# Kernel tuning notes

Measured on AMD Instinct MI355X. Metric: run time of the kernel, lower is better.

The kernel has to match this reference:

```python
import jax, jax.numpy as jnp
import numpy as np

B, D, K = 4096, 512, 64


def setup_inputs() -> dict:
    key = jax.random.key(0)
    k1, k2, k3, k4, k5, k6 = jax.random.split(key, 6)
    observations = jax.random.normal(k1, (B, D), dtype=jnp.float32)
    # binary mask (1 = observed, 0 = missing), stored as float for multiply
    mask = jnp.round(jax.random.uniform(k2, (B, D), dtype=jnp.float32))
    F = jax.random.normal(k3, (1, D, 10), dtype=jnp.float32) * 0.1
    b = jax.random.normal(k4, (1, D, 1), dtype=jnp.float32) * 0.1
    W = jax.random.normal(k5, (11, K), dtype=jnp.float32) * 0.1
    bw = jax.random.normal(k6, (K,), dtype=jnp.float32) * 0.1
    return {"observations": observations, "mask": mask, "F": F, "b": b, "W": W, "bw": bw}


def reference(observations, mask, F, b, W, bw):
    # x_aug per (batch, feature): [x*F_d (10), b_d (1)] -> 11-dim
    Bn = observations.shape[0]
    xF = observations[:, :, None] * F[0]                      # [B, D, 10]
    b_bc = jnp.broadcast_to(b[0], (observations.shape[1], 1)) # [D, 1]
    aug = jnp.concatenate([xF, jnp.broadcast_to(b_bc, (Bn,) + b_bc.shape)], axis=-1)  # [B, D, 11]
    encoded = jnp.einsum('bdf,fk->bdk', aug, W) + bw          # [B, D, K]
    out = jax.nn.relu(jnp.sum(encoded * mask[:, :, None], axis=1))  # [B, K]
    return out
```

## Files before the change

### kernel.cpp

```cpp
#include <hip/hip_runtime.h>
#include <hip/hip_bf16.h>


#define D_DIM 512
#define K_DIM 64
#define B_DIM 4096

typedef __attribute__((ext_vector_type(4))) float f32x4;
typedef __attribute__((ext_vector_type(8))) short bf16x8;

__device__ __forceinline__ unsigned short f2bf(float f) {
    unsigned u = __builtin_bit_cast(unsigned, f);
    u += 0x7fffu + ((u >> 16) & 1u);
    return (unsigned short)(u >> 16);
}

__global__ void prep_Gf_kernel(const float* __restrict__ F,
                               const float* __restrict__ W,
                               unsigned short* __restrict__ Gf) {
    int i = blockIdx.x * blockDim.x + threadIdx.x;
    int lane = i & 63;
    int tp   = (i >> 6) & 15;
    int w    = i >> 10;
    int n     = w * 16 + (lane & 15);
    int dbase = tp * 32 + (lane >> 4) * 8;
    unsigned short v[8];
#pragma unroll
    for (int j = 0; j < 8; ++j) {
        int d = dbase + j;
        float s = 0.f;
#pragma unroll
        for (int f = 0; f < 10; ++f)
            s = fmaf(F[d * 10 + f], W[f * 64 + n], s);
        v[j] = f2bf(s);
    }
    *reinterpret_cast<ushort4*>(Gf + (size_t)i * 8)     = make_ushort4(v[0], v[1], v[2], v[3]);
    *reinterpret_cast<ushort4*>(Gf + (size_t)i * 8 + 4) = make_ushort4(v[4], v[5], v[6], v[7]);
}

__global__ __launch_bounds__(256, 2)
void main_kernel(const float* __restrict__ obs,
                 const float* __restrict__ mask,
                 const float* __restrict__ bvec,
                 const float* __restrict__ W,
                 const float* __restrict__ bw,
                 const unsigned short* __restrict__ Gf,
                 float* __restrict__ out) {
    __shared__ __align__(16) unsigned short Xs[8 * 512];
    __shared__ float s0s[8], s1s[8];

    const int tid  = threadIdx.x;
    const int lane = tid & 63;
    const int w    = tid >> 6;
    const int rowbase = blockIdx.x * 8;

    bf16x8 gfr[16];
#pragma unroll
    for (int tp = 0; tp < 16; ++tp)
        gfr[tp] = *reinterpret_cast<const bf16x8*>(
            Gf + ((size_t)((w * 16 + tp) * 64 + lane)) * 8);

    const int kk = w * 16 + (lane & 15);
    const float w10 = W[10 * K_DIM + kk];
    const float bwv = bw[kk];

    {
        const int r = tid >> 5;
        const int c = tid & 31;
        const float* orow = obs  + (size_t)(rowbase + r) * D_DIM;
        const float* mrow = mask + (size_t)(rowbase + r) * D_DIM;
        f32x4 o[4], m[4], bv[4];
#pragma unroll
        for (int j = 0; j < 4; ++j) {
            int d = c * 4 + 128 * j;
            o[j]  = *reinterpret_cast<const f32x4*>(orow + d);
            m[j]  = *reinterpret_cast<const f32x4*>(mrow + d);
            bv[j] = *reinterpret_cast<const f32x4*>(bvec + d);
        }
        float p0 = 0.f, p1 = 0.f;
        const int swz = r << 4;
        char* xb = reinterpret_cast<char*>(Xs);
#pragma unroll
        for (int j = 0; j < 4; ++j) {
            ushort4 pk;
            pk.x = f2bf(o[j].x * m[j].x);
            pk.y = f2bf(o[j].y * m[j].y);
            pk.z = f2bf(o[j].z * m[j].z);
            pk.w = f2bf(o[j].w * m[j].w);
            int byteoff = r * 1024 + ((c * 8 + 256 * j) ^ swz);
            *reinterpret_cast<ushort4*>(xb + byteoff) = pk;
            p0 += (m[j].x + m[j].y) + (m[j].z + m[j].w);
            p1 = fmaf(m[j].x, bv[j].x, p1);
            p1 = fmaf(m[j].y, bv[j].y, p1);
            p1 = fmaf(m[j].z, bv[j].z, p1);
            p1 = fmaf(m[j].w, bv[j].w, p1);
        }
#pragma unroll
        for (int s = 1; s <= 16; s <<= 1) {
            p0 += __shfl_xor(p0, s, 64);
            p1 += __shfl_xor(p1, s, 64);
        }
        if (c == 0) { s0s[r] = p0; s1s[r] = p1; }
    }
    __syncthreads();

    f32x4 acc = {0.f, 0.f, 0.f, 0.f};
    {
        const int arow = lane & 7;
        const int g    = lane >> 4;
        const char* xb = reinterpret_cast<const char*>(Xs);
#pragma unroll
        for (int tp = 0; tp < 16; ++tp) {
            int byteoff = arow * 1024 + ((64 * tp + 16 * g) ^ (arow << 4));
            bf16x8 a = *reinterpret_cast<const bf16x8*>(xb + byteoff);
            acc = __builtin_amdgcn_mfma_f32_16x16x32_bf16(a, gfr[tp], acc, 0, 0, 0);
        }
    }

    if (lane < 32) {
        const int g = lane >> 4;
#pragma unroll
        for (int r = 0; r < 4; ++r) {
            const int rowl = g * 4 + r;
            float tot = acc[r];
            tot = fmaf(s1s[rowl], w10, tot);
            tot = fmaf(s0s[rowl], bwv, tot);
            out[(size_t)(rowbase + rowl) * K_DIM + kk] = fmaxf(tot, 0.f);
        }
    }
}

extern "C" void kernel_launch(void* const* d_in, const int* in_sizes, int n_in,
                              void* d_out, int out_size, void* d_ws, size_t ws_size,
                              hipStream_t stream) {
    const float* obs  = (const float*)d_in[0];
    const float* mask = (const float*)d_in[1];
    const float* F    = (const float*)d_in[2];
    const float* bvec = (const float*)d_in[3];
    const float* W    = (const float*)d_in[4];
    const float* bw   = (const float*)d_in[5];
    float* out = (float*)d_out;
    unsigned short* Gf = (unsigned short*)d_ws;

    prep_Gf_kernel<<<16, 256, 0, stream>>>(F, W, Gf);
    main_kernel<<<B_DIM / 8, 256, 0, stream>>>(obs, mask, bvec, W, bw, Gf, out);
}
```

Before: 13.16 us.

## Fuse Gf precompute into main kernel using per-block MFMA into LDS

Removes the separate prep kernel launch. Each block now recomputes the F·W product (512x64) itself with small MFMAs and stores it as bf16 in a 64KB LDS buffer. The main MFMA loop then reads its B operand from LDS instead of registers. This saves a launch and a global round-trip, but repeats the precompute in all 512 blocks. The larger LDS footprint may also cut occupancy.

```diff
diff --git a/kernel.cpp b/kernel.cpp
--- a/kernel.cpp
+++ b/kernel.cpp
@@ -14,81 +14,100 @@
     u += 0x7fffu + ((u >> 16) & 1u);
     return (unsigned short)(u >> 16);
 }
-
-__global__ void prep_Gf_kernel(const float* __restrict__ F,
-                               const float* __restrict__ W,
-                               unsigned short* __restrict__ Gf) {
-    int i = blockIdx.x * blockDim.x + threadIdx.x;
-    int lane = i & 63;
-    int tp   = (i >> 6) & 15;
-    int w    = i >> 10;
-    int n     = w * 16 + (lane & 15);
-    int dbase = tp * 32 + (lane >> 4) * 8;
-    unsigned short v[8];
-#pragma unroll
-    for (int j = 0; j < 8; ++j) {
-        int d = dbase + j;
-        float s = 0.f;
-#pragma unroll
-        for (int f = 0; f < 10; ++f)
-            s = fmaf(F[d * 10 + f], W[f * 64 + n], s);
-        v[j] = f2bf(s);
-    }
-    *reinterpret_cast<ushort4*>(Gf + (size_t)i * 8)     = make_ushort4(v[0], v[1], v[2], v[3]);
-    *reinterpret_cast<ushort4*>(Gf + (size_t)i * 8 + 4) = make_ushort4(v[4], v[5], v[6], v[7]);
+__device__ __forceinline__ unsigned pack2(float a, float b) {
+    return (unsigned)f2bf(a) | ((unsigned)f2bf(b) << 16);
 }
 
 __global__ __launch_bounds__(256, 2)
-void main_kernel(const float* __restrict__ obs,
-                 const float* __restrict__ mask,
-                 const float* __restrict__ bvec,
-                 const float* __restrict__ W,
-                 const float* __restrict__ bw,
-                 const unsigned short* __restrict__ Gf,
-                 float* __restrict__ out) {
-    __shared__ __align__(16) unsigned short Xs[8 * 512];
+void fused_kernel(const float* __restrict__ obs,
+                  const float* __restrict__ mask,
+                  const float* __restrict__ bvec,
+                  const float* __restrict__ F,
+                  const float* __restrict__ W,
+                  const float* __restrict__ bw,
+                  float* __restrict__ out) {
+    __shared__ __align__(16) unsigned short GF[4096 * 8];
+    __shared__ __align__(16) unsigned short XF[512 * 8];
     __shared__ float s0s[8], s1s[8];
 
     const int tid  = threadIdx.x;
     const int lane = tid & 63;
     const int w    = tid >> 6;
+    const int ln   = lane & 15;
+    const int g    = lane >> 4;
     const int rowbase = blockIdx.x * 8;
 
-    bf16x8 gfr[16];
+    const int r = tid >> 5;
+    const int c = tid & 31;
+    const float* orow = obs  + (size_t)(rowbase + r) * D_DIM;
+    const float* mrow = mask + (size_t)(rowbase + r) * D_DIM;
+    f32x4 o[4], m[4], bv[4];
 #pragma unroll
-    for (int tp = 0; tp < 16; ++tp)
-        gfr[tp] = *reinterpret_cast<const bf16x8*>(
-            Gf + ((size_t)((w * 16 + tp) * 64 + lane)) * 8);
-
-    const int kk = w * 16 + (lane & 15);
-    const float w10 = W[10 * K_DIM + kk];
-    const float bwv = bw[kk];
+    for (int j = 0; j < 4; ++j) {
+        int d = c * 4 + 128 * j;
+        o[j]  = *reinterpret_cast<const f32x4*>(orow + d);
+        m[j]  = *reinterpret_cast<const f32x4*>(mrow + d);
+        bv[j] = *reinterpret_cast<const f32x4*>(bvec + d);
+    }
 
     {
-        const int r = tid >> 5;
-        const int c = tid & 31;
-        const float* orow = obs  + (size_t)(rowbase + r) * D_DIM;
-        const float* mrow = mask + (size_t)(rowbase + r) * D_DIM;
-        f32x4 o[4], m[4], bv[4];
+        bf16x8 wf[4];
+#pragma unroll
+        for (int nt = 0; nt < 4; ++nt) {
+#pragma unroll
+            for (int j = 0; j < 8; ++j) {
+                int k = g * 8 + j;
+                wf[nt][j] = (k < 10)
+                    ? (short)f2bf(W[k * K_DIM + nt * 16 + ln]) : (short)0;
+            }
+        }
+#pragma unroll
+        for (int i = 0; i < 8; ++i) {
+            const int dt = w * 8 + i;
+            const int Frow = dt * 16 + ln;
+            const float* Fr = F + (size_t)Frow * 10;
+            float fa[8] = {0.f, 0.f, 0.f, 0.f, 0.f, 0.f, 0.f, 0.f};
+            if (g == 0) {
+                float2 t0 = *reinterpret_cast<const float2*>(Fr + 0);
+                float2 t1 = *reinterpret_cast<const float2*>(Fr + 2);
+                float2 t2 = *reinterpret_cast<const float2*>(Fr + 4);
+                float2 t3 = *reinterpret_cast<const float2*>(Fr + 6);
+                fa[0] = t0.x; fa[1] = t0.y; fa[2] = t1.x; fa[3] = t1.y;
+                fa[4] = t2.x; fa[5] = t2.y; fa[6] = t3.x; fa[7] = t3.y;
+            } else if (g == 1) {
+                float2 t = *reinterpret_cast<const float2*>(Fr + 8);
+                fa[0] = t.x; fa[1] = t.y;
+            }
+            bf16x8 af;
+#pragma unroll
+            for (int j = 0; j < 8; ++j) af[j] = (short)f2bf(fa[j]);
+
+#pragma unroll
+            for (int nt = 0; nt < 4; ++nt) {
+                f32x4 gacc = {0.f, 0.f, 0.f, 0.f};
+                gacc = __builtin_amdgcn_mfma_f32_16x16x32_bf16(af, wf[nt], gacc, 0, 0, 0);
+                int slot = (nt * 16 + (dt >> 1)) * 64 + ((dt & 1) * 2 + (g >> 1)) * 16 + ln;
+                uint2 val;
+                val.x = pack2(gacc[0], gacc[1]);
+                val.y = pack2(gacc[2], gacc[3]);
+                *reinterpret_cast<uint2*>(
+                    reinterpret_cast<char*>(GF) + slot * 16 + (g & 1) * 8) = val;
+            }
+        }
+    }
+
+    {
+        float p0 = 0.f, p1 = 0.f;
 #pragma unroll
         for (int j = 0; j < 4; ++j) {
-            int d = c * 4 + 128 * j;
-            o[j]  = *reinterpret_cast<const f32x4*>(orow + d);
-            m[j]  = *reinterpret_cast<const f32x4*>(mrow + d);
-            bv[j] = *reinterpret_cast<const f32x4*>(bvec + d);
-        }
-        float p0 = 0.f, p1 = 0.f;
-        const int swz = r << 4;
-        char* xb = reinterpret_cast<char*>(Xs);
-#pragma unroll
-        for (int j = 0; j < 4; ++j) {
-            ushort4 pk;
-            pk.x = f2bf(o[j].x * m[j].x);
-            pk.y = f2bf(o[j].y * m[j].y);
-            pk.z = f2bf(o[j].z * m[j].z);
-            pk.w = f2bf(o[j].w * m[j].w);
-            int byteoff = r * 1024 + ((c * 8 + 256 * j) ^ swz);
-            *reinterpret_cast<ushort4*>(xb + byteoff) = pk;
+            uint2 xv;
+            xv.x = pack2(o[j].x * m[j].x, o[j].y * m[j].y);
+            xv.y = pack2(o[j].z * m[j].z, o[j].w * m[j].w);
+            int tp   = (c >> 3) + 4 * j;
+            int gch  = (c >> 1) & 3;
+            int slot = r * 64 + ((tp * 4 + gch) ^ r);
+            *reinterpret_cast<uint2*>(
+                reinterpret_cast<char*>(XF) + slot * 16 + (c & 1) * 8) = xv;
             p0 += (m[j].x + m[j].y) + (m[j].z + m[j].w);
             p1 = fmaf(m[j].x, bv[j].x, p1);
             p1 = fmaf(m[j].y, bv[j].y, p1);
@@ -107,22 +126,26 @@
     f32x4 acc = {0.f, 0.f, 0.f, 0.f};
     {
         const int arow = lane & 7;
-        const int g    = lane >> 4;
-        const char* xb = reinterpret_cast<const char*>(Xs);
+        const char* xb = reinterpret_cast<const char*>(XF);
+        const char* gb = reinterpret_cast<const char*>(GF);
 #pragma unroll
         for (int tp = 0; tp < 16; ++tp) {
-            int byteoff = arow * 1024 + ((64 * tp + 16 * g) ^ (arow << 4));
-            bf16x8 a = *reinterpret_cast<const bf16x8*>(xb + byteoff);
-            acc = __builtin_amdgcn_mfma_f32_16x16x32_bf16(a, gfr[tp], acc, 0, 0, 0);
+            bf16x8 a = *reinterpret_cast<const bf16x8*>(
+                xb + (arow * 64 + ((tp * 4 + g) ^ arow)) * 16);
+            bf16x8 b = *reinterpret_cast<const bf16x8*>(
+                gb + ((w * 16 + tp) * 64 + lane) * 16);
+            acc = __builtin_amdgcn_mfma_f32_16x16x32_bf16(a, b, acc, 0, 0, 0);
         }
     }
 
+    const int kk = w * 16 + ln;
     if (lane < 32) {
-        const int g = lane >> 4;
+        const float w10 = W[10 * K_DIM + kk];
+        const float bwv = bw[kk];
 #pragma unroll
-        for (int r = 0; r < 4; ++r) {
-            const int rowl = g * 4 + r;
-            float tot = acc[r];
+        for (int rr = 0; rr < 4; ++rr) {
+            const int rowl = g * 4 + rr;
+            float tot = acc[rr];
             tot = fmaf(s1s[rowl], w10, tot);
             tot = fmaf(s0s[rowl], bwv, tot);
             out[(size_t)(rowbase + rowl) * K_DIM + kk] = fmaxf(tot, 0.f);
@@ -140,8 +163,6 @@
     const float* W    = (const float*)d_in[4];
     const float* bw   = (const float*)d_in[5];
     float* out = (float*)d_out;
-    unsigned short* Gf = (unsigned short*)d_ws;
 
-    prep_Gf_kernel<<<16, 256, 0, stream>>>(F, W, Gf);
-    main_kernel<<<B_DIM / 8, 256, 0, stream>>>(obs, mask, bvec, W, bw, Gf, out);
+    fused_kernel<<<B_DIM / 8, 256, 0, stream>>>(obs, mask, bvec, F, W, bw, out);
 }
```

Result: slower. 15.13 us (+14.9%).
